# Kernel optimization log

Hardware: AMD Instinct MI355X
Metric: run time of the kernel (lower is better)

Reference implementation:

```python
import jax, jax.numpy as jnp
import numpy as np

B, N, DIM, H, DH, MLP, L = 4, 1024, 1024, 16, 64, 4096, 2
C = DIM // 4  # conditioning dim = 256


def setup_inputs() -> dict:
    key = jax.random.key(0)
    ks = jax.random.split(key, 12)
    s = 0.02
    return dict(
        x=jax.random.normal(ks[0], (B, N, DIM), jnp.float32),
        mu=jax.random.normal(ks[1], (B, N, C), jnp.float32),
        f=jax.random.normal(ks[2], (B, N, C), jnp.float32),
        Wqkv=jax.random.normal(ks[3], (L, DIM, 3 * H * DH), jnp.float32) * s,
        Wout=jax.random.normal(ks[4], (L, H * DH, DIM), jnp.float32) * s,
        bout=jnp.zeros((L, DIM), jnp.float32),
        W1=jax.random.normal(ks[5], (L, DIM, MLP), jnp.float32) * s,
        b1=jnp.zeros((L, MLP), jnp.float32),
        W2=jax.random.normal(ks[6], (L, MLP, DIM), jnp.float32) * s,
        b2=jnp.zeros((L, DIM), jnp.float32),
        Wmu=jax.random.normal(ks[7], (L, C, 6 * C), jnp.float32) * s,
        bmu=jnp.zeros((L, 6 * C), jnp.float32),
        Wf=jax.random.normal(ks[8], (L, C, 6 * 3 * C), jnp.float32) * s,
        bf=jnp.zeros((L, 6 * 3 * C), jnp.float32),
        g1=jnp.ones((L, DIM), jnp.float32),
        be1=jnp.zeros((L, DIM), jnp.float32),
        g2=jnp.ones((L, DIM), jnp.float32),
        be2=jnp.zeros((L, DIM), jnp.float32),
    )


def _ln(x, g, b):
    m = jnp.mean(x, -1, keepdims=True)
    v = jnp.mean((x - m) ** 2, -1, keepdims=True)
    return (x - m) * jax.lax.rsqrt(v + 1e-5) * g + b


def reference(x, mu, f, Wqkv, Wout, bout, W1, b1, W2, b2, Wmu, bmu, Wf, bf, g1, be1, g2, be2):
    scale = DH ** -0.5
    smu = jax.nn.silu(mu)  # SiLU applied to raw conditioning, shared across layers
    sf = jax.nn.silu(f)
    for i in range(L):
        mm = smu @ Wmu[i] + bmu[i]          # [B,N,6*C]
        mf = sf @ Wf[i] + bf[i]             # [B,N,6*3*C]
        mus = jnp.split(mm, 6, axis=-1)     # each [B,N,C]
        fs = jnp.split(mf, 6, axis=-1)      # each [B,N,3C]
        sh_a, sc_a, ga_a, sh_m, sc_m, ga_m = [
            jnp.concatenate([a, b_], -1) for a, b_ in zip(mus, fs)
        ]                                   # each [B,N,DIM]
        # attention branch
        h = _ln(x, g1[i], be1[i]) * (1 + sc_a) + sh_a
        qkv = h @ Wqkv[i]                   # [B,N,3*H*DH]
        q, k, v = [t.reshape(B, N, H, DH) for t in jnp.split(qkv, 3, axis=-1)]
        att = jax.nn.softmax(jnp.einsum('bihd,bjhd->bhij', q, k) * scale, axis=-1)
        o = jnp.einsum('bhij,bjhd->bihd', att, v).reshape(B, N, H * DH)
        x = x + ga_a * (o @ Wout[i] + bout[i])
        # MLP branch
        h2 = _ln(x, g2[i], be2[i]) * (1 + sc_m) + sh_m
        mlp = jax.nn.gelu(h2 @ W1[i] + b1[i], approximate=False) @ W2[i] + b2[i]
        x = x + ga_m * mlp
    return x
```

## Files before the change

kernel.cpp:

```cpp
#include <hip/hip_runtime.h>
#include <math.h>

#define BB 4
#define NN 1024
#define DIMD 1024
#define HHN 16
#define DHH 64
#define MLPD 4096
#define LLN 2
#define CCD 256
#define BNROWS (BB*NN)
#define NSPLIT 4

typedef __attribute__((ext_vector_type(8))) _Float16 h8;
typedef __attribute__((ext_vector_type(4))) _Float16 h4;
typedef __attribute__((ext_vector_type(4))) float f32x4;

#define GLD16(gp, lp) __builtin_amdgcn_global_load_lds( \
    (const __attribute__((address_space(1))) void*)(gp), \
    (__attribute__((address_space(3))) void*)(lp), 16, 0, 0)

__global__ __launch_bounds__(256) void silu_kernel(const float* __restrict__ in,
                                                   _Float16* __restrict__ out, int n4) {
  int i = blockIdx.x * 256 + threadIdx.x;
  if (i < n4) {
    float4 v = ((const float4*)in)[i];
    h4 o;
    o[0] = (_Float16)(v.x / (1.f + __expf(-v.x)));
    o[1] = (_Float16)(v.y / (1.f + __expf(-v.y)));
    o[2] = (_Float16)(v.z / (1.f + __expf(-v.z)));
    o[3] = (_Float16)(v.w / (1.f + __expf(-v.w)));
    ((h4*)out)[i] = o;
  }
}

__global__ __launch_bounds__(256) void transpose_cast(const float* __restrict__ in,
                                                      _Float16* __restrict__ out,
                                                      int K, int N) {
  __shared__ float tile[64][68];
  int bx = blockIdx.x * 64;
  int by = blockIdx.y * 64;
  int tid = threadIdx.x;
  int r0 = tid >> 4, c4 = (tid & 15) * 4;
  #pragma unroll
  for (int i = 0; i < 4; i++) {
    float4 v = *(const float4*)(in + (size_t)(by + r0 + i * 16) * N + bx + c4);
    *(float4*)&tile[r0 + i * 16][c4] = v;
  }
  __syncthreads();
  #pragma unroll
  for (int i = 0; i < 4; i++) {
    int orow = r0 + i * 16;
    h4 o;
    #pragma unroll
    for (int j = 0; j < 4; j++) o[j] = (_Float16)tile[c4 + j][orow];
    *(h4*)(out + (size_t)(bx + orow) * K + by + c4) = o;
  }
}

__global__ __launch_bounds__(256) void v_transpose(const _Float16* __restrict__ qkv,
                                                   _Float16* __restrict__ vt) {
  __shared__ _Float16 t[64][72];
  int n0 = blockIdx.x * 64;
  int bh = blockIdx.y;
  int b = bh >> 4;
  const _Float16* src = qkv + (size_t)b * NN * 3072 + 2048 + (bh & 15) * 64;
  int tid = threadIdx.x;
  int row = tid >> 2, c0 = (tid & 3) * 16;
  *(h8*)&t[row][c0] = *(const h8*)(src + (size_t)(n0 + row) * 3072 + c0);
  *(h8*)&t[row][c0 + 8] = *(const h8*)(src + (size_t)(n0 + row) * 3072 + c0 + 8);
  __syncthreads();
  int d = tid >> 2, ns = (tid & 3) * 16;
  h8 o0, o1;
  #pragma unroll
  for (int j = 0; j < 8; j++) { o0[j] = t[ns + j][d]; o1[j] = t[ns + 8 + j][d]; }
  _Float16* dst = vt + ((size_t)bh * 64 + d) * NN + n0 + ns;
  *(h8*)dst = o0;
  *(h8*)(dst + 8) = o1;
}

template <int EPI>
__global__ __launch_bounds__(256) void gemm128(
    const _Float16* __restrict__ A, const _Float16* __restrict__ Bt,
    int M, int Nt, int Ktot, int Kper,
    const float* __restrict__ bias, _Float16* __restrict__ outp) {
  __shared__ _Float16 As[2][128 * 32];
  __shared__ _Float16 Bs[2][128 * 32];
  const int tid = threadIdx.x;
  const int wave = tid >> 6, lane = tid & 63;
  const int brow = blockIdx.x * 128, bcol = blockIdx.y * 128;
  const size_t kbase = (size_t)blockIdx.z * Kper;
  const int wr = (wave >> 1) * 64, wc = (wave & 1) * 64;
  const int r = lane & 15, g = lane >> 4;
  f32x4 acc[4][4];
  #pragma unroll
  for (int m = 0; m < 4; m++)
    #pragma unroll
    for (int n = 0; n < 4; n++) acc[m][n] = (f32x4){0.f, 0.f, 0.f, 0.f};

  const int scol = ((lane & 3) ^ ((lane >> 3) & 3)) * 8;
  const _Float16* gA = A + (size_t)(brow + wave * 32 + (lane >> 2)) * Ktot + kbase + scol;
  const _Float16* gB = Bt + (size_t)(bcol + wave * 32 + (lane >> 2)) * Ktot + kbase + scol;

  auto STAGE = [&](int slot, int k0) {
    GLD16(gA + k0, &As[slot][wave * 1024]);
    GLD16(gA + k0 + 16 * (size_t)Ktot, &As[slot][wave * 1024 + 512]);
    GLD16(gB + k0, &Bs[slot][wave * 1024]);
    GLD16(gB + k0 + 16 * (size_t)Ktot, &Bs[slot][wave * 1024 + 512]);
  };

  const int NT = Kper / 32;
  STAGE(0, 0);
  const int gg = g ^ ((r >> 1) & 3);
  int cur = 0;
  for (int t = 0; t < NT; ++t) {
    __syncthreads();
    if (t + 1 < NT) STAGE(cur ^ 1, (t + 1) * 32);
    h8 af[4], bf[4];
    #pragma unroll
    for (int m = 0; m < 4; m++) af[m] = *(const h8*)(&As[cur][(wr + m * 16 + r) * 32 + gg * 8]);
    #pragma unroll
    for (int n = 0; n < 4; n++) bf[n] = *(const h8*)(&Bs[cur][(wc + n * 16 + r) * 32 + gg * 8]);
    #pragma unroll
    for (int m = 0; m < 4; m++)
      #pragma unroll
      for (int n = 0; n < 4; n++)
        acc[m][n] = __builtin_amdgcn_mfma_f32_16x16x32_f16(bf[n], af[m], acc[m][n], 0, 0, 0);
    cur ^= 1;
  }

  #pragma unroll
  for (int m = 0; m < 4; m++) {
    const int grow = brow + wr + m * 16 + r;
    #pragma unroll
    for (int n = 0; n < 4; n++) {
      const int gcol = bcol + wc + n * 16 + 4 * g;
      float4 bv4 = (EPI != 2 && bias) ? *(const float4*)(bias + gcol)
                                      : float4{0.f, 0.f, 0.f, 0.f};
      float v[4] = {acc[m][n][0] + bv4.x, acc[m][n][1] + bv4.y,
                    acc[m][n][2] + bv4.z, acc[m][n][3] + bv4.w};
      h4 o;
      if (EPI == 1) {
        #pragma unroll
        for (int q = 0; q < 4; q++)
          o[q] = (_Float16)(0.5f * v[q] * (1.f + erff(v[q] * 0.70710678118f)));
      } else {
        #pragma unroll
        for (int q = 0; q < 4; q++) o[q] = (_Float16)v[q];
      }
      _Float16* dst = (EPI == 2)
          ? outp + (size_t)blockIdx.z * M * Nt + (size_t)grow * Nt + gcol
          : outp + (size_t)grow * Nt + gcol;
      *(h4*)dst = o;
    }
  }
}

__global__ __launch_bounds__(256) void ln_mod_res(
    float* __restrict__ x,
    const _Float16* __restrict__ parts, const float* __restrict__ dbias,
    const _Float16* __restrict__ mga, const _Float16* __restrict__ fga, int jga,
    const _Float16* __restrict__ msc, const _Float16* __restrict__ fsc, int jsh, int jsc,
    const float* __restrict__ gam, const float* __restrict__ bet,
    _Float16* __restrict__ hout) {
  const int row = blockIdx.x;
  const int tid = threadIdx.x;
  const int c0 = tid * 4;
  float* xr = x + (size_t)row * DIMD;
  float4 v = *(float4*)(xr + c0);
  if (parts) {
    float4 db = *(const float4*)(dbias + c0);
    float d[4] = {db.x, db.y, db.z, db.w};
    #pragma unroll
    for (int s = 0; s < NSPLIT; s++) {
      h4 p = *(const h4*)(parts + (size_t)s * BNROWS * DIMD + (size_t)row * DIMD + c0);
      #pragma unroll
      for (int i = 0; i < 4; i++) d[i] += (float)p[i];
    }
    h4 g4 = (c0 < CCD)
        ? *(const h4*)(mga + (size_t)row * (6 * CCD) + jga * CCD + c0)
        : *(const h4*)(fga + (size_t)row * (18 * CCD) + jga * (3 * CCD) + (c0 - CCD));
    v.x += (float)g4[0] * d[0];
    v.y += (float)g4[1] * d[1];
    v.z += (float)g4[2] * d[2];
    v.w += (float)g4[3] * d[3];
    *(float4*)(xr + c0) = v;
  }
  float s = v.x + v.y + v.z + v.w;
  float sq = v.x * v.x + v.y * v.y + v.z * v.z + v.w * v.w;
  #pragma unroll
  for (int off = 32; off > 0; off >>= 1) {
    s += __shfl_down(s, off);
    sq += __shfl_down(sq, off);
  }
  __shared__ float red[8];
  int wv = tid >> 6, ln = tid & 63;
  if (ln == 0) { red[wv] = s; red[4 + wv] = sq; }
  __syncthreads();
  s = red[0] + red[1] + red[2] + red[3];
  sq = red[4] + red[5] + red[6] + red[7];
  float mean = s * (1.f / DIMD);
  float var = sq * (1.f / DIMD) - mean * mean;
  float rs = rsqrtf(var + 1e-5f);
  float4 gm = *(const float4*)(gam + c0);
  float4 bt = *(const float4*)(bet + c0);
  h4 sh4 = (c0 < CCD)
      ? *(const h4*)(msc + (size_t)row * (6 * CCD) + jsh * CCD + c0)
      : *(const h4*)(fsc + (size_t)row * (18 * CCD) + jsh * (3 * CCD) + (c0 - CCD));
  h4 sc4 = (c0 < CCD)
      ? *(const h4*)(msc + (size_t)row * (6 * CCD) + jsc * CCD + c0)
      : *(const h4*)(fsc + (size_t)row * (18 * CCD) + jsc * (3 * CCD) + (c0 - CCD));
  float xv[4] = {v.x, v.y, v.z, v.w};
  float gv[4] = {gm.x, gm.y, gm.z, gm.w};
  float bv[4] = {bt.x, bt.y, bt.z, bt.w};
  h4 o;
  #pragma unroll
  for (int i = 0; i < 4; i++) {
    float lnv = (xv[i] - mean) * rs * gv[i] + bv[i];
    o[i] = (_Float16)(lnv * (1.f + (float)sc4[i]) + (float)sh4[i]);
  }
  *((h4*)(hout + (size_t)row * DIMD + c0)) = o;
}

__global__ __launch_bounds__(256) void res_final(
    float* __restrict__ x,
    const _Float16* __restrict__ parts, const float* __restrict__ dbias,
    const _Float16* __restrict__ mga, const _Float16* __restrict__ fga, int jga) {
  const int row = blockIdx.x;
  const int c0 = threadIdx.x * 4;
  float* xr = x + (size_t)row * DIMD;
  float4 v = *(float4*)(xr + c0);
  float4 db = *(const float4*)(dbias + c0);
  float d[4] = {db.x, db.y, db.z, db.w};
  #pragma unroll
  for (int s = 0; s < NSPLIT; s++) {
    h4 p = *(const h4*)(parts + (size_t)s * BNROWS * DIMD + (size_t)row * DIMD + c0);
    #pragma unroll
    for (int i = 0; i < 4; i++) d[i] += (float)p[i];
  }
  h4 g4 = (c0 < CCD)
      ? *(const h4*)(mga + (size_t)row * (6 * CCD) + jga * CCD + c0)
      : *(const h4*)(fga + (size_t)row * (18 * CCD) + jga * (3 * CCD) + (c0 - CCD));
  v.x += (float)g4[0] * d[0];
  v.y += (float)g4[1] * d[1];
  v.z += (float)g4[2] * d[2];
  v.w += (float)g4[3] * d[3];
  *(float4*)(xr + c0) = v;
}

__global__ __launch_bounds__(256) void attn_kernel(const _Float16* __restrict__ qkv,
                                                   const _Float16* __restrict__ vt,
                                                   _Float16* __restrict__ o) {
  __shared__ _Float16 Ks[2 * 64 * 64];
  __shared__ _Float16 Vs[2 * 64 * 64];
  __shared__ _Float16 Ps[4][32 * 72];
  const int bhg = blockIdx.x * 8 + (blockIdx.y & 7);
  const int qt = blockIdx.y >> 3;
  const int b = bhg >> 4, hh = bhg & 15;
  const int tid = threadIdx.x;
  const int wave = tid >> 6, lane = tid & 63;
  const int r = lane & 15, g = lane >> 4;
  const int RS = 3 * HHN * DHH;
  const _Float16* qb = qkv + (size_t)b * NN * RS + hh * DHH;
  const _Float16* kb = qb + HHN * DHH;
  const _Float16* vtb = vt + (size_t)bhg * DHH * NN;
  const int q0 = qt * 128 + wave * 32;

  h8 qf[2][2];
  #pragma unroll
  for (int m = 0; m < 2; m++) {
    qf[m][0] = *(const h8*)(qb + (size_t)(q0 + m * 16 + r) * RS + g * 8);
    qf[m][1] = *(const h8*)(qb + (size_t)(q0 + m * 16 + r) * RS + 32 + g * 8);
  }

  f32x4 oacc[2][4];
  #pragma unroll
  for (int m = 0; m < 2; m++)
    #pragma unroll
    for (int n = 0; n < 4; n++) oacc[m][n] = (f32x4){0.f, 0.f, 0.f, 0.f};
  float mrun[2][4], lrun[2][4];
  #pragma unroll
  for (int m = 0; m < 2; m++)
    #pragma unroll
    for (int q = 0; q < 4; q++) { mrun[m][q] = -1e30f; lrun[m][q] = 0.f; }
  const float scale = 0.125f;
  _Float16* Pw = Ps[wave];

  auto STAGE = [&](int buf, int k0) {
    #pragma unroll
    for (int i = 0; i < 2; i++) {
      int chunk = wave * 2 + i;
      int blk = chunk * 64 + lane;
      int row = blk >> 3, c16 = blk & 7;
      int sc = ((c16 ^ (row & 7))) * 8;
      GLD16(kb + (size_t)(k0 + row) * RS + sc, Ks + buf * 4096 + chunk * 512);
      GLD16(vtb + (size_t)row * NN + k0 + sc, Vs + buf * 4096 + chunk * 512);
    }
  };

  STAGE(0, 0);
  int cur = 0;
  for (int kt = 0; kt < NN / 64; ++kt) {
    __syncthreads();
    if (kt + 1 < NN / 64) STAGE(cur ^ 1, (kt + 1) * 64);
    const _Float16* Kb = Ks + cur * 4096;
    const _Float16* Vb = Vs + cur * 4096;
    f32x4 sfr[2][4];
    #pragma unroll
    for (int m = 0; m < 2; m++)
      #pragma unroll
      for (int n = 0; n < 4; n++) sfr[m][n] = (f32x4){0.f, 0.f, 0.f, 0.f};
    #pragma unroll
    for (int n = 0; n < 4; n++) {
      int row = n * 16 + r, sw = row & 7;
      h8 kf0 = *(const h8*)(Kb + row * 64 + (g ^ sw) * 8);
      h8 kf1 = *(const h8*)(Kb + row * 64 + ((4 + g) ^ sw) * 8);
      #pragma unroll
      for (int m = 0; m < 2; m++) {
        sfr[m][n] = __builtin_amdgcn_mfma_f32_16x16x32_f16(qf[m][0], kf0, sfr[m][n], 0, 0, 0);
        sfr[m][n] = __builtin_amdgcn_mfma_f32_16x16x32_f16(qf[m][1], kf1, sfr[m][n], 0, 0, 0);
      }
    }
    #pragma unroll
    for (int m = 0; m < 2; m++) {
      float pm[4];
      #pragma unroll
      for (int q = 0; q < 4; q++)
        pm[q] = fmaxf(fmaxf(sfr[m][0][q], sfr[m][1][q]), fmaxf(sfr[m][2][q], sfr[m][3][q])) * scale;
      #pragma unroll
      for (int off = 1; off < 16; off <<= 1)
        #pragma unroll
        for (int q = 0; q < 4; q++) pm[q] = fmaxf(pm[q], __shfl_xor(pm[q], off));
      float fac[4], rsum[4];
      #pragma unroll
      for (int q = 0; q < 4; q++) {
        float mn = fmaxf(mrun[m][q], pm[q]);
        fac[q] = __expf(mrun[m][q] - mn);
        mrun[m][q] = mn;
        rsum[q] = 0.f;
      }
      #pragma unroll
      for (int n = 0; n < 4; n++)
        #pragma unroll
        for (int q = 0; q < 4; q++) {
          float p = __expf(sfr[m][n][q] * scale - mrun[m][q]);
          sfr[m][n][q] = p;
          rsum[q] += p;
        }
      #pragma unroll
      for (int off = 1; off < 16; off <<= 1)
        #pragma unroll
        for (int q = 0; q < 4; q++) rsum[q] += __shfl_xor(rsum[q], off);
      #pragma unroll
      for (int q = 0; q < 4; q++) lrun[m][q] = lrun[m][q] * fac[q] + rsum[q];
      #pragma unroll
      for (int n = 0; n < 4; n++)
        #pragma unroll
        for (int q = 0; q < 4; q++) oacc[m][n][q] *= fac[q];
      #pragma unroll
      for (int n = 0; n < 4; n++)
        #pragma unroll
        for (int q = 0; q < 4; q++)
          Pw[(m * 16 + 4 * g + q) * 72 + n * 16 + r] = (_Float16)sfr[m][n][q];
    }
    h8 pa[2][2];
    #pragma unroll
    for (int m = 0; m < 2; m++) {
      pa[m][0] = *(const h8*)(Pw + (m * 16 + r) * 72 + g * 8);
      pa[m][1] = *(const h8*)(Pw + (m * 16 + r) * 72 + 32 + g * 8);
    }
    #pragma unroll
    for (int nd = 0; nd < 4; nd++) {
      int row = nd * 16 + r, sw = row & 7;
      h8 vf0 = *(const h8*)(Vb + row * 64 + (g ^ sw) * 8);
      h8 vf1 = *(const h8*)(Vb + row * 64 + ((4 + g) ^ sw) * 8);
      #pragma unroll
      for (int m = 0; m < 2; m++) {
        oacc[m][nd] = __builtin_amdgcn_mfma_f32_16x16x32_f16(pa[m][0], vf0, oacc[m][nd], 0, 0, 0);
        oacc[m][nd] = __builtin_amdgcn_mfma_f32_16x16x32_f16(pa[m][1], vf1, oacc[m][nd], 0, 0, 0);
      }
    }
    cur ^= 1;
  }
  #pragma unroll
  for (int m = 0; m < 2; m++)
    #pragma unroll
    for (int nd = 0; nd < 4; nd++)
      #pragma unroll
      for (int q = 0; q < 4; q++) {
        int row = q0 + m * 16 + 4 * g + q;
        int col = hh * DHH + nd * 16 + r;
        o[((size_t)b * NN + row) * DIMD + col] = (_Float16)(oacc[m][nd][q] / lrun[m][q]);
      }
}

extern "C" void kernel_launch(void* const* d_in, const int* in_sizes, int n_in,
                              void* d_out, int out_size, void* d_ws, size_t ws_size,
                              hipStream_t stream) {
  (void)in_sizes; (void)n_in; (void)out_size; (void)ws_size;
  const float* mu   = (const float*)d_in[1];
  const float* f_in = (const float*)d_in[2];
  const float* Wqkv = (const float*)d_in[3];
  const float* Wout = (const float*)d_in[4];
  const float* bout = (const float*)d_in[5];
  const float* W1   = (const float*)d_in[6];
  const float* b1   = (const float*)d_in[7];
  const float* W2   = (const float*)d_in[8];
  const float* b2   = (const float*)d_in[9];
  const float* Wmu  = (const float*)d_in[10];
  const float* bmu  = (const float*)d_in[11];
  const float* Wf   = (const float*)d_in[12];
  const float* bfv  = (const float*)d_in[13];
  const float* g1   = (const float*)d_in[14];
  const float* be1  = (const float*)d_in[15];
  const float* g2   = (const float*)d_in[16];
  const float* be2  = (const float*)d_in[17];
  float* xout = (float*)d_out;

  char* ws = (char*)d_ws;
  size_t off = 0;
  auto alloc = [&](size_t elems) -> _Float16* {
    _Float16* p = (_Float16*)(ws + off);
    off += ((elems * 2 + 255) / 256) * 256;
    return p;
  };
  _Float16* wTqkv = alloc((size_t)LLN * 3072 * 1024);
  _Float16* wTout = alloc((size_t)LLN * 1024 * 1024);
  _Float16* wT1   = alloc((size_t)LLN * 4096 * 1024);
  _Float16* wT2   = alloc((size_t)LLN * 1024 * 4096);
  _Float16* wTmu  = alloc((size_t)LLN * 1536 * 256);
  _Float16* wTf   = alloc((size_t)LLN * 4608 * 256);
  _Float16* smu   = alloc((size_t)BNROWS * CCD);
  _Float16* sfb   = alloc((size_t)BNROWS * CCD);
  _Float16* mmb[2] = {alloc((size_t)BNROWS * 6 * CCD), alloc((size_t)BNROWS * 6 * CCD)};
  _Float16* mfb[2] = {alloc((size_t)BNROWS * 18 * CCD), alloc((size_t)BNROWS * 18 * CCD)};
  _Float16* hbuf  = alloc((size_t)BNROWS * DIMD);
  _Float16* obuf  = alloc((size_t)BNROWS * DIMD);
  _Float16* m1b   = alloc((size_t)BNROWS * MLPD);
  _Float16* region = alloc((size_t)NSPLIT * BNROWS * DIMD);
  _Float16* qkvb  = region;
  _Float16* vtb   = region + (size_t)BNROWS * 3 * DIMD;
  _Float16* parts = region;

  hipMemcpyAsync(d_out, d_in[0], (size_t)BNROWS * DIMD * sizeof(float),
                 hipMemcpyDeviceToDevice, stream);

  silu_kernel<<<BNROWS * CCD / 4 / 256, 256, 0, stream>>>(mu, smu, BNROWS * CCD / 4);
  silu_kernel<<<BNROWS * CCD / 4 / 256, 256, 0, stream>>>(f_in, sfb, BNROWS * CCD / 4);

  for (int l = 0; l < LLN; l++) {
    transpose_cast<<<dim3(3072 / 64, 1024 / 64), 256, 0, stream>>>(
        Wqkv + (size_t)l * 1024 * 3072, wTqkv + (size_t)l * 3072 * 1024, 1024, 3072);
    transpose_cast<<<dim3(1024 / 64, 1024 / 64), 256, 0, stream>>>(
        Wout + (size_t)l * 1024 * 1024, wTout + (size_t)l * 1024 * 1024, 1024, 1024);
    transpose_cast<<<dim3(4096 / 64, 1024 / 64), 256, 0, stream>>>(
        W1 + (size_t)l * 1024 * 4096, wT1 + (size_t)l * 4096 * 1024, 1024, 4096);
    transpose_cast<<<dim3(1024 / 64, 4096 / 64), 256, 0, stream>>>(
        W2 + (size_t)l * 4096 * 1024, wT2 + (size_t)l * 1024 * 4096, 4096, 1024);
    transpose_cast<<<dim3(1536 / 64, 256 / 64), 256, 0, stream>>>(
        Wmu + (size_t)l * 256 * 1536, wTmu + (size_t)l * 1536 * 256, 256, 1536);
    transpose_cast<<<dim3(4608 / 64, 256 / 64), 256, 0, stream>>>(
        Wf + (size_t)l * 256 * 4608, wTf + (size_t)l * 4608 * 256, 256, 4608);
  }

  for (int l = 0; l < LLN; l++) {
    gemm128<0><<<dim3(BNROWS / 128, 1536 / 128), 256, 0, stream>>>(
        smu, wTmu + (size_t)l * 1536 * 256, BNROWS, 1536, 256, 256,
        bmu + (size_t)l * 1536, mmb[l]);
    gemm128<0><<<dim3(BNROWS / 128, 4608 / 128), 256, 0, stream>>>(
        sfb, wTf + (size_t)l * 4608 * 256, BNROWS, 4608, 256, 256,
        bfv + (size_t)l * 4608, mfb[l]);
    ln_mod_res<<<BNROWS, 256, 0, stream>>>(
        xout, (l == 0) ? nullptr : parts,
        (l == 0) ? nullptr : b2 + (size_t)(l - 1) * DIMD,
        mmb[l ^ 1], mfb[l ^ 1], 5,
        mmb[l], mfb[l], 0, 1,
        g1 + (size_t)l * DIMD, be1 + (size_t)l * DIMD, hbuf);
    gemm128<0><<<dim3(BNROWS / 128, 3072 / 128), 256, 0, stream>>>(
        hbuf, wTqkv + (size_t)l * 3072 * 1024, BNROWS, 3072, 1024, 1024,
        nullptr, qkvb);
    v_transpose<<<dim3(NN / 64, BB * HHN), 256, 0, stream>>>(qkvb, vtb);
    attn_kernel<<<dim3(NN / 128, BB * HHN), 256, 0, stream>>>(qkvb, vtb, obuf);
    gemm128<2><<<dim3(BNROWS / 128, 1024 / 128, NSPLIT), 256, 0, stream>>>(
        obuf, wTout + (size_t)l * 1024 * 1024, BNROWS, 1024, 1024, 1024 / NSPLIT,
        nullptr, parts);
    ln_mod_res<<<BNROWS, 256, 0, stream>>>(
        xout, parts, bout + (size_t)l * DIMD,
        mmb[l], mfb[l], 2,
        mmb[l], mfb[l], 3, 4,
        g2 + (size_t)l * DIMD, be2 + (size_t)l * DIMD, hbuf);
    gemm128<1><<<dim3(BNROWS / 128, 4096 / 128), 256, 0, stream>>>(
        hbuf, wT1 + (size_t)l * 4096 * 1024, BNROWS, 4096, 1024, 1024,
        b1 + (size_t)l * MLPD, m1b);
    gemm128<2><<<dim3(BNROWS / 128, 1024 / 128, NSPLIT), 256, 0, stream>>>(
        m1b, wT2 + (size_t)l * 1024 * 4096, BNROWS, 1024, 4096, 4096 / NSPLIT,
        nullptr, parts);
  }
  res_final<<<BNROWS, 256, 0, stream>>>(
      xout, parts, b2 + (size_t)(LLN - 1) * DIMD, mmb[(LLN - 1) & 1], mfb[(LLN - 1) & 1], 5);
}
```

Measured before the change: 720.4 us.

## Add 256x256-tile 4-stage pipelined GEMM for the large projections

```diff
diff --git a/kernel.cpp b/kernel.cpp
--- a/kernel.cpp
+++ b/kernel.cpp
@@ -77,6 +77,100 @@
   _Float16* dst = vt + ((size_t)bh * 64 + d) * NN + n0 + ns;
   *(h8*)dst = o0;
   *(h8*)(dst + 8) = o1;
+}
+
+template <int EPI>
+__global__ __launch_bounds__(512, 2) void gemm256(
+    const _Float16* __restrict__ A, const _Float16* __restrict__ Bt,
+    int M, int Nt, int Ktot, int Kper,
+    const float* __restrict__ bias, _Float16* __restrict__ outp) {
+  __shared__ _Float16 As[4][256 * 32];
+  __shared__ _Float16 Bs[4][256 * 32];
+  const int tid = threadIdx.x;
+  const int wave = tid >> 6, lane = tid & 63;
+  const int brow = blockIdx.x * 256, bcol = blockIdx.y * 256;
+  const size_t kbase = (size_t)blockIdx.z * Kper;
+  const int wr = (wave >> 2) * 128, wc = (wave & 3) * 64;
+  const int r = lane & 15, g = lane >> 4;
+  f32x4 acc[8][4];
+  #pragma unroll
+  for (int m = 0; m < 8; m++)
+    #pragma unroll
+    for (int n = 0; n < 4; n++) acc[m][n] = (f32x4){0.f, 0.f, 0.f, 0.f};
+
+  const int arow = lane >> 2;
+  const int scol = ((lane & 3) ^ ((lane >> 3) & 3)) * 8;
+  const _Float16* gA = A + (size_t)(brow + wave * 32 + arow) * Ktot + kbase + scol;
+  const _Float16* gB = Bt + (size_t)(bcol + wave * 32 + arow) * Ktot + kbase + scol;
+
+  auto STAGE = [&](int sl, int s) {
+    const size_t ko = (size_t)s * 32;
+    #pragma unroll
+    for (int j = 0; j < 2; j++) {
+      GLD16(gA + ko + (size_t)j * 16 * Ktot, &As[sl][(wave * 32 + j * 16) * 32]);
+      GLD16(gB + ko + (size_t)j * 16 * Ktot, &Bs[sl][(wave * 32 + j * 16) * 32]);
+    }
+  };
+
+  const int NS = Kper / 32;
+  #pragma unroll
+  for (int s = 0; s < 4; ++s)
+    if (s < NS) STAGE(s, s);
+
+  const int gg = g ^ ((r >> 1) & 3);
+
+  for (int s = 0; s < NS; ++s) {
+    const int sl = s & 3;
+    const int rem = NS - 1 - s;
+    if (rem >= 3)      asm volatile("s_waitcnt vmcnt(12)" ::: "memory");
+    else if (rem == 2) asm volatile("s_waitcnt vmcnt(8)" ::: "memory");
+    else if (rem == 1) asm volatile("s_waitcnt vmcnt(4)" ::: "memory");
+    else               asm volatile("s_waitcnt vmcnt(0)" ::: "memory");
+    __builtin_amdgcn_s_barrier();
+    asm volatile("" ::: "memory");
+    h8 af[8], bf[4];
+    #pragma unroll
+    for (int m = 0; m < 8; m++)
+      af[m] = *(const h8*)(&As[sl][(wr + m * 16 + r) * 32 + gg * 8]);
+    #pragma unroll
+    for (int n = 0; n < 4; n++)
+      bf[n] = *(const h8*)(&Bs[sl][(wc + n * 16 + r) * 32 + gg * 8]);
+    #pragma unroll
+    for (int m = 0; m < 8; m++)
+      #pragma unroll
+      for (int n = 0; n < 4; n++)
+        acc[m][n] = __builtin_amdgcn_mfma_f32_16x16x32_f16(bf[n], af[m], acc[m][n], 0, 0, 0);
+    asm volatile("s_waitcnt lgkmcnt(0)" ::: "memory");
+    __builtin_amdgcn_s_barrier();
+    asm volatile("" ::: "memory");
+    if (s + 4 < NS) STAGE(sl, s + 4);
+  }
+
+  #pragma unroll
+  for (int m = 0; m < 8; m++) {
+    const int grow = brow + wr + m * 16 + r;
+    #pragma unroll
+    for (int n = 0; n < 4; n++) {
+      const int gcol = bcol + wc + n * 16 + 4 * g;
+      float4 bv4 = (EPI != 2 && bias) ? *(const float4*)(bias + gcol)
+                                      : float4{0.f, 0.f, 0.f, 0.f};
+      float v[4] = {acc[m][n][0] + bv4.x, acc[m][n][1] + bv4.y,
+                    acc[m][n][2] + bv4.z, acc[m][n][3] + bv4.w};
+      h4 o;
+      if (EPI == 1) {
+        #pragma unroll
+        for (int q = 0; q < 4; q++)
+          o[q] = (_Float16)(0.5f * v[q] * (1.f + erff(v[q] * 0.70710678118f)));
+      } else {
+        #pragma unroll
+        for (int q = 0; q < 4; q++) o[q] = (_Float16)v[q];
+      }
+      _Float16* dst = (EPI == 2)
+          ? outp + (size_t)blockIdx.z * M * Nt + (size_t)grow * Nt + gcol
+          : outp + (size_t)grow * Nt + gcol;
+      *(h4*)dst = o;
+    }
+  }
 }
 
 template <int EPI>
@@ -476,12 +570,12 @@
         mmb[l ^ 1], mfb[l ^ 1], 5,
         mmb[l], mfb[l], 0, 1,
         g1 + (size_t)l * DIMD, be1 + (size_t)l * DIMD, hbuf);
-    gemm128<0><<<dim3(BNROWS / 128, 3072 / 128), 256, 0, stream>>>(
+    gemm256<0><<<dim3(BNROWS / 256, 3072 / 256), 512, 0, stream>>>(
         hbuf, wTqkv + (size_t)l * 3072 * 1024, BNROWS, 3072, 1024, 1024,
         nullptr, qkvb);
     v_transpose<<<dim3(NN / 64, BB * HHN), 256, 0, stream>>>(qkvb, vtb);
     attn_kernel<<<dim3(NN / 128, BB * HHN), 256, 0, stream>>>(qkvb, vtb, obuf);
-    gemm128<2><<<dim3(BNROWS / 128, 1024 / 128, NSPLIT), 256, 0, stream>>>(
+    gemm256<2><<<dim3(BNROWS / 256, 1024 / 256, NSPLIT), 512, 0, stream>>>(
         obuf, wTout + (size_t)l * 1024 * 1024, BNROWS, 1024, 1024, 1024 / NSPLIT,
         nullptr, parts);
     ln_mod_res<<<BNROWS, 256, 0, stream>>>(
@@ -489,10 +583,10 @@
         mmb[l], mfb[l], 2,
         mmb[l], mfb[l], 3, 4,
         g2 + (size_t)l * DIMD, be2 + (size_t)l * DIMD, hbuf);
-    gemm128<1><<<dim3(BNROWS / 128, 4096 / 128), 256, 0, stream>>>(
+    gemm256<1><<<dim3(BNROWS / 256, 4096 / 256), 512, 0, stream>>>(
         hbuf, wT1 + (size_t)l * 4096 * 1024, BNROWS, 4096, 1024, 1024,
         b1 + (size_t)l * MLPD, m1b);
-    gemm128<2><<<dim3(BNROWS / 128, 1024 / 128, NSPLIT), 256, 0, stream>>>(
+    gemm256<2><<<dim3(BNROWS / 256, 1024 / 256, NSPLIT), 512, 0, stream>>>(
         m1b, wT2 + (size_t)l * 1024 * 4096, BNROWS, 1024, 4096, 4096 / NSPLIT,
         nullptr, parts);
   }
```

New measurement: 708.7 us. About the same (-1.6%).
